# Kernel tuning notes

Hardware: AMD Instinct MI355X
Metric: run time of the kernel (lower is better)

## Reference

```python
import jax, jax.numpy as jnp
import numpy as np

W = 5; WW = 25; STEP = 8; DF = 128; NH = 8; DH = 16; EPS = 1e-5


def sinusoid_pe(ww, d):
    pos = np.arange(ww)[:, None].astype(np.float32)
    div = np.exp(np.arange(0, d, 2).astype(np.float32) * (-np.log(10000.0) / d))
    pe = np.zeros((ww, d), np.float32)
    pe[:, 0::2] = np.sin(pos * div)
    pe[:, 1::2] = np.cos(pos * div)
    return jnp.asarray(pe)


def ln(x, s, b):
    m = x.mean(-1, keepdims=True)
    v = ((x - m) ** 2).mean(-1, keepdims=True)
    return (x - m) / jnp.sqrt(v + EPS) * s + b


def attn_layer(x, src, wq, wk, wv, wm, m1w, m1b, m2w, m2b, n1s, n1b, n2s, n2b):
    N, T, D = x.shape
    q = (x @ wq).reshape(N, T, NH, DH)
    k = (src @ wk).reshape(N, T, NH, DH)
    v = (src @ wv).reshape(N, T, NH, DH)
    a = jax.nn.softmax(jnp.einsum('nqhd,nkhd->nhqk', q, k) * (DH ** -0.5), axis=-1)
    msg = jnp.einsum('nhqk,nkhd->nqhd', a, v).reshape(N, T, D) @ wm
    msg = ln(msg, n1s, n1b)
    h = jnp.concatenate([x, msg], axis=-1)
    h = jax.nn.relu(h @ m1w + m1b) @ m2w + m2b
    return x + ln(h, n2s, n2b)


def local_transformer(x0, x1, P):
    names = ['self', 'cross', 'self', 'cross']
    for i, nm in enumerate(names):
        p = tuple(a[i] for a in P)
        if nm == 'self':
            x0 = attn_layer(x0, x0, *p)
            x1 = attn_layer(x1, x1, *p)
        else:
            x0 = attn_layer(x0, x1, *p)
            x1 = attn_layer(x1, x0, *p)
    return x0, x1


def unfold_window(fm):
    # F.unfold(kernel=5, stride=4, pad=2) then 'B (C MM) L -> B L MM C'
    B, C, H, Wd = fm.shape
    pat = jax.lax.conv_general_dilated_patches(fm, (W, W), (4, 4), [(W // 2, W // 2)] * 2)
    Ho, Wo = pat.shape[2], pat.shape[3]
    pat = pat.reshape(B, C, WW, Ho * Wo)  # channel-major ordering matches torch unfold
    return pat.transpose(0, 3, 2, 1)  # [B, L, WW, C]


def forward(mdesc0, mdesc1, fine0, fine1, conv_w, conv_b, proj_w, proj_b,
            merge_w, merge_b, reg1_w, reg1_b, reg2_w, reg2_b, reg_w, reg_b,
            lt_wq, lt_wk, lt_wv, lt_wm, lt_m1w, lt_m1b, lt_m2w, lt_m2b,
            lt_n1s, lt_n1b, lt_n2s, lt_n2b):
    B, L, Dc = mdesc0.shape
    Wc = int(np.sqrt(L))
    # dual-softmax confidence matrix
    sim = jnp.einsum('bld,bmd->blm', mdesc0 / Dc, mdesc1 / Dc) / 0.1
    cm = jax.nn.softmax(sim, axis=1) * jax.nn.softmax(sim, axis=2)
    # mutual nearest-neighbor filter (static-shape: keep all B*L rows + mask)
    mut = (cm == cm.max(axis=2, keepdims=True)) & (cm == cm.max(axis=1, keepdims=True))
    cf = cm * mut
    mask = cf.max(axis=2) > 0  # [B, L]
    j = jnp.argmax(cf, axis=2)  # [B, L]
    # 1x1 conv to fine dim
    f0 = jnp.einsum('bchw,oc->bohw', fine0, conv_w[:, :, 0, 0]) + conv_b[None, :, None, None]
    f1 = jnp.einsum('bchw,oc->bohw', fine1, conv_w[:, :, 0, 0]) + conv_b[None, :, None, None]
    u0 = unfold_window(f0)
    u1 = unfold_window(f1)  # [B, L, WW, DF]
    N = B * L
    b_all = jnp.repeat(jnp.arange(B), L)
    idx1 = b_all * L + j.reshape(-1)
    local0 = u0.reshape(N, WW, DF)
    local1 = u1.reshape(N, WW, DF)[idx1]
    c0 = mdesc0.reshape(N, Dc)
    c1 = mdesc1.reshape(N, Dc)[idx1]
    local = jnp.concatenate([local0, local1], axis=0)  # [2N, WW, DF]
    center = jnp.concatenate([c0, c1], axis=0) @ proj_w + proj_b  # [2N, DF]
    center = jnp.broadcast_to(center[:, None, :], (2 * N, WW, DF))
    ld = jnp.concatenate([local, center], axis=-1) @ merge_w + merge_b
    ld = ld + sinusoid_pe(WW, DF)[None]
    d0, d1 = ld[:N], ld[N:]
    P = (lt_wq, lt_wk, lt_wv, lt_wm, lt_m1w, lt_m1b, lt_m2w, lt_m2b, lt_n1s, lt_n1b, lt_n2s, lt_n2b)
    fd0, fd1 = local_transformer(d0, d1, P)
    c = WW // 2
    cen = jnp.broadcast_to(fd0[:, c:c + 1, :], (N, WW, DF))
    feat = jnp.concatenate([cen, fd1], axis=-1)  # [N, WW, 2*DF]
    feat = feat @ reg1_w + reg1_b  # [N, WW, DF]
    feat = feat.reshape(N, WW * DF)  # [N, 3200]
    feat = feat @ reg2_w + reg2_b  # dropout is identity at eval
    coords = feat @ reg_w + reg_b  # [N, 2]
    xj = (j % Wc) * STEP
    yj = (j // Wc) * STEP
    base = jnp.stack([xj, yj], axis=-1).reshape(N, 2).astype(coords.dtype)
    return (base + coords) * mask.reshape(N, 1).astype(coords.dtype)


def setup_inputs():
    key = jax.random.key(0)
    ks = jax.random.split(key, 24)
    B, L, Dc = 2, 2304, 256
    Hf = 192
    nl = 4

    def rn(k, shape, fan):
        return jax.random.normal(k, shape, jnp.float32) * (fan ** -0.5)

    return {
        'mdesc0': jax.random.normal(ks[0], (B, L, Dc), jnp.float32),
        'mdesc1': jax.random.normal(ks[1], (B, L, Dc), jnp.float32),
        'fine0': jax.random.normal(ks[2], (B, Dc, Hf, Hf), jnp.float32),
        'fine1': jax.random.normal(ks[3], (B, Dc, Hf, Hf), jnp.float32),
        'conv_w': rn(ks[4], (DF, Dc, 1, 1), Dc),
        'conv_b': jnp.zeros((DF,), jnp.float32),
        'proj_w': rn(ks[5], (Dc, DF), Dc),
        'proj_b': jnp.zeros((DF,), jnp.float32),
        'merge_w': rn(ks[6], (2 * DF, DF), 2 * DF),
        'merge_b': jnp.zeros((DF,), jnp.float32),
        'reg1_w': rn(ks[7], (2 * DF, DF), 2 * DF),
        'reg1_b': jnp.zeros((DF,), jnp.float32),
        'reg2_w': rn(ks[8], (WW * DF, DF), WW * DF),
        'reg2_b': jnp.zeros((DF,), jnp.float32),
        'reg_w': rn(ks[9], (DF, 2), DF),
        'reg_b': jnp.zeros((2,), jnp.float32),
        'lt_wq': rn(ks[10], (nl, DF, DF), DF),
        'lt_wk': rn(ks[11], (nl, DF, DF), DF),
        'lt_wv': rn(ks[12], (nl, DF, DF), DF),
        'lt_wm': rn(ks[13], (nl, DF, DF), DF),
        'lt_m1w': rn(ks[14], (nl, 2 * DF, 2 * DF), 2 * DF),
        'lt_m1b': jnp.zeros((nl, 2 * DF), jnp.float32),
        'lt_m2w': rn(ks[15], (nl, 2 * DF, DF), 2 * DF),
        'lt_m2b': jnp.zeros((nl, DF), jnp.float32),
        'lt_n1s': jnp.ones((nl, DF), jnp.float32),
        'lt_n1b': jnp.zeros((nl, DF), jnp.float32),
        'lt_n2s': jnp.ones((nl, DF), jnp.float32),
        'lt_n2b': jnp.zeros((nl, DF), jnp.float32),
    }


def reference(mdesc0, mdesc1, fine0, fine1, conv_w, conv_b, proj_w, proj_b,
              merge_w, merge_b, reg1_w, reg1_b, reg2_w, reg2_b, reg_w, reg_b,
              lt_wq, lt_wk, lt_wv, lt_wm, lt_m1w, lt_m1b, lt_m2w, lt_m2b,
              lt_n1s, lt_n1b, lt_n2s, lt_n2b):
    return forward(mdesc0, mdesc1, fine0, fine1, conv_w, conv_b, proj_w, proj_b,
                   merge_w, merge_b, reg1_w, reg1_b, reg2_w, reg2_b, reg_w, reg_b,
                   lt_wq, lt_wk, lt_wv, lt_wm, lt_m1w, lt_m1b, lt_m2w, lt_m2b,
                   lt_n1s, lt_n1b, lt_n2s, lt_n2b)
```

## Files before the change

kernel.cpp:

```cpp
#include <hip/hip_runtime.h>
#include <stdint.h>
#include <type_traits>

#define DEVFN static __device__ __forceinline__

typedef __attribute__((ext_vector_type(8))) short bf16x8v;
typedef __attribute__((ext_vector_type(4))) float f32x4v;
typedef __attribute__((ext_vector_type(2))) _Float16 h2;

DEVFN float b2f(short s) {
  union { unsigned u; float f; } c; c.u = ((unsigned)(unsigned short)s) << 16; return c.f;
}
DEVFN short f2b(float f) {
  union { float f; unsigned u; } c; c.f = f;
  unsigned r = c.u + 0x7fffu + ((c.u >> 16) & 1u);
  return (short)(r >> 16);
}
DEVFN short f2h(float f) {
  union { _Float16 h; short s; } c; c.h = (_Float16)f; return c.s;
}
DEVFN void gl_lds16(const void* g, void* l) {
  __builtin_amdgcn_global_load_lds((const __attribute__((address_space(1))) void*)g,
                                   (__attribute__((address_space(3))) void*)l, 16, 0, 0);
}
DEVFN double exp_small(double x) {
  return 1.0 + x * (1.0 + x * (0.5 + x * ((1.0 / 6.0) + x * (1.0 / 24.0))));
}


__global__ void prep_all(const float* __restrict__ conv_w, const float* __restrict__ proj_w,
                         const float* __restrict__ merge_w, const float* __restrict__ reg1_w,
                         const float* __restrict__ reg2_w, const float* __restrict__ wq,
                         const float* __restrict__ wk, const float* __restrict__ wv,
                         const float* __restrict__ wm, const float* __restrict__ m1w,
                         const float* __restrict__ m2w,
                         short* __restrict__ convT, short* __restrict__ projT,
                         short* __restrict__ mergeAT, short* __restrict__ mergeBT,
                         short* __restrict__ reg1T, short* __restrict__ reg2T,
                         short* __restrict__ wqkvT, short* __restrict__ wmT,
                         short* __restrict__ m1T, short* __restrict__ m2T,
                         float* __restrict__ pe, short* __restrict__ zp) {
  const int L0 = 32768, L1 = 32768, L2 = 16384, L3 = 16384, L4 = 32768, L5 = 409600;
  const int L6 = 196608, L7 = 65536, L8 = 262144, L9 = 131072, L10 = 3200, L11 = 128;
  const int TOT = L0+L1+L2+L3+L4+L5+L6+L7+L8+L9+L10+L11;
  for (int gi = blockIdx.x * blockDim.x + threadIdx.x; gi < TOT; gi += gridDim.x * blockDim.x) {
    int i = gi;
    if (i < L0) { convT[i] = f2b(conv_w[i]); continue; } i -= L0;
    if (i < L1) { int n = i >> 8, k = i & 255; projT[i] = f2b(proj_w[k * 128 + n]); continue; } i -= L1;
    if (i < L2) { int n = i >> 7, k = i & 127; mergeAT[i] = f2b(merge_w[k * 128 + n]); continue; } i -= L2;
    if (i < L3) { int n = i >> 7, k = i & 127; mergeBT[i] = f2b(merge_w[(128 + k) * 128 + n]); continue; } i -= L3;
    if (i < L4) { int n = i >> 8, k = i & 255; reg1T[i] = f2b(reg1_w[k * 128 + n]); continue; } i -= L4;
    if (i < L5) { int n = i / 3200, k = i - n * 3200; reg2T[i] = f2b(reg2_w[k * 128 + n]); continue; } i -= L5;
    if (i < L6) {
      int l = i / 49152; int r = i - l * 49152; int w = r / 16384; int r2 = r - w * 16384;
      int n = r2 >> 7, k = r2 & 127;
      const float* s = (w == 0) ? wq : (w == 1) ? wk : wv;
      wqkvT[i] = f2b(s[l * 16384 + k * 128 + n]); continue;
    } i -= L6;
    if (i < L7) { int l = i >> 14; int r = i & 16383; int n = r >> 7, k = r & 127;
      wmT[i] = f2b(wm[l * 16384 + k * 128 + n]); continue; } i -= L7;
    if (i < L8) { int l = i >> 16; int r = i & 65535; int n = r >> 8, k = r & 255;
      m1T[i] = f2b(m1w[l * 65536 + k * 256 + n]); continue; } i -= L8;
    if (i < L9) { int l = i >> 15; int r = i & 32767; int n = r >> 8, k = r & 255;
      m2T[i] = f2b(m2w[l * 32768 + k * 128 + n]); continue; } i -= L9;
    if (i < L10) {
      int t = i >> 7, d = i & 127; int i2 = d >> 1;
      float div = expf(((float)(2 * i2)) * (-logf(10000.f) / 128.f));
      float ang = (float)t * div;
      pe[i] = (d & 1) ? cosf(ang) : sinf(ang); continue;
    } i -= L10;
    zp[i] = 0;
  }
}


__global__ __launch_bounds__(256) void sim_gemm(const float* __restrict__ A,
                                                const float* __restrict__ Bm,
                                                float* __restrict__ S) {
  int b = blockIdx.z;
  A += (size_t)b * 2304 * 256; Bm += (size_t)b * 2304 * 256; S += (size_t)b * 2304 * 2304;
  __shared__ float As[96][33], Bs[96][33];
  int tid = threadIdx.x;
  int tx = tid & 15, ty = tid >> 4;
  int rb = blockIdx.x * 96, cb = blockIdx.y * 96;
  float acc[6][6] = {};
  for (int k0 = 0; k0 < 256; k0 += 32) {
    #pragma unroll
    for (int s = 0; s < 3; ++s) {
      int slot = s * 256 + tid;
      int r = slot >> 3, cq = slot & 7;
      float4 va = *(const float4*)&A[(size_t)(rb + r) * 256 + k0 + 4 * cq];
      float4 vb = *(const float4*)&Bm[(size_t)(cb + r) * 256 + k0 + 4 * cq];
      As[r][4 * cq] = va.x; As[r][4 * cq + 1] = va.y; As[r][4 * cq + 2] = va.z; As[r][4 * cq + 3] = va.w;
      Bs[r][4 * cq] = vb.x; Bs[r][4 * cq + 1] = vb.y; Bs[r][4 * cq + 2] = vb.z; Bs[r][4 * cq + 3] = vb.w;
    }
    __syncthreads();
    #pragma unroll 4
    for (int k = 0; k < 32; ++k) {
      float av[6], bv[6];
      #pragma unroll
      for (int i = 0; i < 6; ++i) av[i] = As[ty + 16 * i][k];
      #pragma unroll
      for (int j = 0; j < 6; ++j) bv[j] = Bs[tx + 16 * j][k];
      #pragma unroll
      for (int i = 0; i < 6; ++i)
        #pragma unroll
        for (int j = 0; j < 6; ++j) acc[i][j] += av[i] * bv[j];
    }
    __syncthreads();
  }
  #pragma unroll
  for (int i = 0; i < 6; ++i)
    #pragma unroll
    for (int j = 0; j < 6; ++j) {
      float t = acc[i][j] * (1.0f / 65536.0f);
      S[(size_t)(rb + ty + 16 * i) * 2304 + cb + tx + 16 * j] = t / 0.1f;
    }
}

__global__ __launch_bounds__(256) void row_lse(const float* __restrict__ S, double* __restrict__ lnR) {
  int row = blockIdx.x;
  const float* Sp = S + (size_t)row * 2304;
  double a = 0;
  for (int m = threadIdx.x; m < 2304; m += 256) a += exp_small((double)Sp[m]);
  __shared__ double red[256];
  red[threadIdx.x] = a; __syncthreads();
  for (int s = 128; s > 0; s >>= 1) { if (threadIdx.x < (unsigned)s) red[threadIdx.x] += red[threadIdx.x + s]; __syncthreads(); }
  if (!threadIdx.x) lnR[row] = log(red[0]);
}

__global__ __launch_bounds__(256) void col_part(const float* __restrict__ S,
                                                const double* __restrict__ lnR,
                                                double* __restrict__ psum,
                                                double* __restrict__ pkey,
                                                int* __restrict__ pidx) {
  int bb = blockIdx.z;
  int c0 = blockIdx.x * 64;
  int rc = blockIdx.y;
  int col = c0 + (threadIdx.x & 63);
  int g = threadIdx.x >> 6;
  const float* Sp = S + (size_t)bb * 2304 * 2304;
  const double* lr = lnR + bb * 2304;
  double a = 0, best = -1e300; int bi = 1 << 30;
  int l0 = rc * 192;
  for (int t = g; t < 192; t += 4) {
    int l = l0 + t;
    double sv = (double)Sp[(size_t)l * 2304 + col];
    a += exp_small(sv);
    double k = 2.0 * sv - lr[l];
    if (k > best || (k == best && l < bi)) { best = k; bi = l; }
  }
  __shared__ double s_sum[256]; __shared__ double s_key[256]; __shared__ int s_idx[256];
  s_sum[threadIdx.x] = a; s_key[threadIdx.x] = best; s_idx[threadIdx.x] = bi;
  __syncthreads();
  if (g == 0) {
    double ts = a; double tk = best; int ti = bi;
    #pragma unroll
    for (int gg = 1; gg < 4; ++gg) {
      int o = threadIdx.x + gg * 64;
      ts += s_sum[o];
      if (s_key[o] > tk || (s_key[o] == tk && s_idx[o] < ti)) { tk = s_key[o]; ti = s_idx[o]; }
    }
    size_t off = ((size_t)bb * 12 + rc) * 2304 + col;
    psum[off] = ts; pkey[off] = tk; pidx[off] = ti;
  }
}

__global__ void col_reduce(const double* __restrict__ psum, const double* __restrict__ pkey,
                           const int* __restrict__ pidx, double* __restrict__ lnC,
                           int* __restrict__ CB) {
  int i = blockIdx.x * blockDim.x + threadIdx.x;
  if (i >= 4608) return;
  int bb = i / 2304, col = i - bb * 2304;
  double s = 0; double bk = -1e300; int bi = 1 << 30;
  for (int rc = 0; rc < 12; ++rc) {
    size_t off = ((size_t)bb * 12 + rc) * 2304 + col;
    s += psum[off];
    double k = pkey[off]; int ix = pidx[off];
    if (k > bk || (k == bk && ix < bi)) { bk = k; bi = ix; }
  }
  lnC[i] = log(s);
  CB[i] = bi;
}

__global__ __launch_bounds__(256) void row_argmax(const float* __restrict__ S,
                                                  const double* __restrict__ lnC,
                                                  int* __restrict__ J) {
  int row = blockIdx.x; int bb = row / 2304;
  const float* Sp = S + (size_t)row * 2304;
  const double* lc = lnC + bb * 2304;
  double best = -1e300; int bi = 1 << 30;
  for (int m = threadIdx.x; m < 2304; m += 256) {
    double k = 2.0 * (double)Sp[m] - lc[m];
    if (k > best || (k == best && m < bi)) { best = k; bi = m; }
  }
  __shared__ double bvs[256]; __shared__ int bis[256];
  bvs[threadIdx.x] = best; bis[threadIdx.x] = bi; __syncthreads();
  for (int s = 128; s > 0; s >>= 1) {
    if (threadIdx.x < (unsigned)s) {
      double ov = bvs[threadIdx.x + s]; int oi = bis[threadIdx.x + s];
      if (ov > bvs[threadIdx.x] || (ov == bvs[threadIdx.x] && oi < bis[threadIdx.x])) { bvs[threadIdx.x] = ov; bis[threadIdx.x] = oi; }
    }
    __syncthreads();
  }
  if (!threadIdx.x) J[row] = bis[0];
}


__global__ __launch_bounds__(256) void transpose_fine(const float* __restrict__ src, short* __restrict__ dst) {
  __shared__ float t[64][65];
  int bb = blockIdx.z, p0 = blockIdx.x * 64, c0 = blockIdx.y * 64;
  for (int i = threadIdx.x; i < 4096; i += 256) {
    int cl = i >> 6, pl = i & 63;
    t[cl][pl] = src[((size_t)(bb * 256 + c0 + cl)) * 36864 + p0 + pl];
  }
  __syncthreads();
  for (int i = threadIdx.x; i < 1024; i += 256) {
    int pl = i >> 4, cg = (i & 15) * 4;
    unsigned w0 = (unsigned short)f2b(t[cg][pl]) | ((unsigned)(unsigned short)f2b(t[cg + 1][pl]) << 16);
    unsigned w1 = (unsigned short)f2b(t[cg + 2][pl]) | ((unsigned)(unsigned short)f2b(t[cg + 3][pl]) << 16);
    int2 v; v.x = (int)w0; v.y = (int)w1;
    *(int2*)&dst[((size_t)(bb * 36864 + p0 + pl)) * 256 + c0 + cg] = v;
  }
}

__global__ void cgather(const float* __restrict__ md0, const float* __restrict__ md1,
                        const int* __restrict__ J, short* __restrict__ cbuf) {
  int total = 9216 * 256;
  for (int i = blockIdx.x * blockDim.x + threadIdx.x; i < total; i += gridDim.x * blockDim.x) {
    int w = i >> 8, c = i & 255;
    const float* src;
    if (w < 4608) src = md0 + (size_t)w * 256;
    else {
      int n = w - 4608; int bb = n / 2304;
      src = md1 + (size_t)(bb * 2304 + J[n]) * 256;
    }
    cbuf[i] = f2b(src[c]);
  }
}

__global__ void build_tab(const int* __restrict__ J, const short* __restrict__ f0c,
                          const short* __restrict__ f1c, const short* __restrict__ zp,
                          unsigned long long* __restrict__ tab) {
  int total = 230400;
  for (int i = blockIdx.x * blockDim.x + threadIdx.x; i < total; i += gridDim.x * blockDim.x) {
    int w = i / 25, t = i - w * 25;
    int bb, cell; const short* fc;
    if (w < 4608) { bb = w / 2304; cell = w - bb * 2304; fc = f0c; }
    else { int n = w - 4608; bb = n / 2304; cell = J[n]; fc = f1c; }
    int cy = cell / 48, cx = cell - cy * 48;
    int y = cy * 4 - 2 + t / 5, x = cx * 4 - 2 + t % 5;
    const short* p = (y >= 0 && y < 192 && x >= 0 && x < 192)
                   ? fc + (size_t)((bb * 192 + y) * 192 + x) * 128 : zp;
    tab[i] = (unsigned long long)(uintptr_t)p;
  }
}


constexpr int AM_LIN = 0, AM_DUAL = 1, AM_TAB = 2, AM_CEN = 3, AM_QKV = 4;
constexpr int EP_BIAS = 0, EP_BF32 = 1, EP_RELU = 2, EP_LN = 3, EP_LNRES = 4, EP_MERGE = 5, EP_PART = 6, EP_F16 = 7;

template<int AMODE, int EPI>
__global__ __launch_bounds__(256)
void gemm_bf16(const short* __restrict__ A1, const short* __restrict__ A2,
               const unsigned long long* __restrict__ tab,
               const short* __restrict__ Wt, int M, int Kd, int kstr, int K1,
               const float* __restrict__ bias, int bstride,
               const float* __restrict__ lns, const float* __restrict__ lnb,
               const short* __restrict__ resid,
               const float* __restrict__ ccp, const float* __restrict__ pep,
               short* __restrict__ outb, float* __restrict__ outf, int ldc,
               long wstride, long ostride) {
  __shared__ __align__(16) short As[128 * 64];
  __shared__ __align__(16) short Bs[128 * 64];
  __shared__ float rsum[2][128], rsq[2][128];
  int tid = threadIdx.x, lane = tid & 63, wid = tid >> 6;
  int wr = wid >> 1, wc = wid & 1;
  int nwg = gridDim.x;
  int orig = blockIdx.x;
  int qd = nwg >> 3, rm = nwg & 7;
  int xcd = orig & 7, offx = orig >> 3;
  int bx = (xcd < rm ? xcd * (qd + 1) : rm * (qd + 1) + (xcd - rm) * qd) + offx;
  int rb = bx * 128;
  int by = blockIdx.y;
  int koff = blockIdx.z * Kd;
  const short* Wsel = Wt + (size_t)by * wstride;
  const float* bsel = bias ? bias + (size_t)by * bstride : nullptr;
  short* osel_b = outb ? outb + (size_t)by * ostride : nullptr;
  float* osel_f = outf ? outf + (size_t)by * ostride : nullptr;

  f32x4v acc[4][4];
  #pragma unroll
  for (int i = 0; i < 4; ++i)
    #pragma unroll
    for (int j = 0; j < 4; ++j) acc[i][j] = (f32x4v){0.f, 0.f, 0.f, 0.f};

  for (int k0 = 0; k0 < Kd; k0 += 64) {
    #pragma unroll
    for (int q = 0; q < 4; ++q) {
      int i = (wid * 4 + q) * 64 + lane;
      int r = i >> 3, pch = i & 7;
      int c = pch ^ (r & 7);
      const short* src;
      if (AMODE == AM_LIN) {
        src = A1 + (size_t)(rb + r) * kstr + koff + k0 + c * 8;
      } else if (AMODE == AM_QKV) {
        const short* Ab = (by == 0) ? A1 : A2;
        src = Ab + (size_t)(rb + r) * kstr + k0 + c * 8;
      } else if (AMODE == AM_DUAL) {
        if (k0 < K1) src = A1 + (size_t)(rb + r) * K1 + k0 + c * 8;
        else         src = A2 + (size_t)(rb + r) * (Kd - K1) + (k0 - K1) + c * 8;
      } else if (AMODE == AM_CEN) {
        int rg = rb + r;
        if (k0 < K1) src = A1 + (size_t)((rg / 25) * 25 + 12) * K1 + k0 + c * 8;
        else         src = A2 + (size_t)rg * (Kd - K1) + (k0 - K1) + c * 8;
      } else {
        src = (const short*)(uintptr_t)tab[rb + r] + k0 + c * 8;
      }
      gl_lds16(src, &As[(size_t)i * 8]);
    }
    #pragma unroll
    for (int q = 0; q < 4; ++q) {
      int i = (wid * 4 + q) * 64 + lane;
      int r = i >> 3, pch = i & 7;
      int c = pch ^ (r & 7);
      gl_lds16(Wsel + (size_t)r * kstr + koff + k0 + c * 8, &Bs[(size_t)i * 8]);
    }
    __syncthreads();
    #pragma unroll
    for (int kk = 0; kk < 2; ++kk) {
      bf16x8v af[4], bfr[4];
      #pragma unroll
      for (int mi = 0; mi < 4; ++mi) {
        int r = wr * 64 + mi * 16 + (lane & 15);
        int c = kk * 4 + (lane >> 4);
        int pch = c ^ (r & 7);
        af[mi] = *(const bf16x8v*)&As[r * 64 + pch * 8];
      }
      #pragma unroll
      for (int ni = 0; ni < 4; ++ni) {
        int r = wc * 64 + ni * 16 + (lane & 15);
        int c = kk * 4 + (lane >> 4);
        int pch = c ^ (r & 7);
        bfr[ni] = *(const bf16x8v*)&Bs[r * 64 + pch * 8];
      }
      #pragma unroll
      for (int mi = 0; mi < 4; ++mi)
        #pragma unroll
        for (int ni = 0; ni < 4; ++ni)
          acc[mi][ni] = __builtin_amdgcn_mfma_f32_16x16x32_bf16(af[mi], bfr[ni], acc[mi][ni], 0, 0, 0);
    }
    __syncthreads();
  }

  int colloc[4];
  #pragma unroll
  for (int ni = 0; ni < 4; ++ni) colloc[ni] = wc * 64 + ni * 16 + (lane & 15);
  float bv[4];
  #pragma unroll
  for (int ni = 0; ni < 4; ++ni)
    bv[ni] = (EPI == EP_MERGE || EPI == EP_PART) ? 0.f : (bsel ? bsel[colloc[ni]] : 0.f);

  #pragma unroll
  for (int mi = 0; mi < 4; ++mi)
    #pragma unroll
    for (int ni = 0; ni < 4; ++ni)
      #pragma unroll
      for (int q = 0; q < 4; ++q) {
        float v = acc[mi][ni][q] + bv[ni];
        if (EPI == EP_RELU) v = fmaxf(v, 0.f);
        acc[mi][ni][q] = v;
      }

  if (EPI == EP_LN || EPI == EP_LNRES) {
    #pragma unroll
    for (int mi = 0; mi < 4; ++mi)
      #pragma unroll
      for (int q = 0; q < 4; ++q) {
        float s = 0.f, ss = 0.f;
        #pragma unroll
        for (int ni = 0; ni < 4; ++ni) { float v = acc[mi][ni][q]; s += v; ss += v * v; }
        s += __shfl_xor(s, 1, 64); ss += __shfl_xor(ss, 1, 64);
        s += __shfl_xor(s, 2, 64); ss += __shfl_xor(ss, 2, 64);
        s += __shfl_xor(s, 4, 64); ss += __shfl_xor(ss, 4, 64);
        s += __shfl_xor(s, 8, 64); ss += __shfl_xor(ss, 8, 64);
        int rl = wr * 64 + mi * 16 + (lane >> 4) * 4 + q;
        if ((lane & 15) == 0) { rsum[wc][rl] = s; rsq[wc][rl] = ss; }
      }
    __syncthreads();
  }

  #pragma unroll
  for (int mi = 0; mi < 4; ++mi)
    #pragma unroll
    for (int q = 0; q < 4; ++q) {
      int rl = wr * 64 + mi * 16 + (lane >> 4) * 4 + q;
      long rg = rb + rl;
      float mean = 0.f, rstd = 0.f;
      if (EPI == EP_LN || EPI == EP_LNRES) {
        float s = rsum[0][rl] + rsum[1][rl];
        float ss = rsq[0][rl] + rsq[1][rl];
        mean = s * (1.f / 128.f);
        float var = ss * (1.f / 128.f) - mean * mean;
        rstd = 1.f / sqrtf(var + 1e-5f);
      }
      int wv_ = 0, tv_ = 0;
      if (EPI == EP_MERGE) { wv_ = (int)(rg / 25); tv_ = (int)(rg - (long)wv_ * 25); }
      #pragma unroll
      for (int ni = 0; ni < 4; ++ni) {
        int cg = colloc[ni];
        float v = acc[mi][ni][q];
        if (EPI == EP_MERGE) v += ccp[(size_t)wv_ * 128 + cg] + pep[tv_ * 128 + cg];
        if (EPI == EP_LN || EPI == EP_LNRES) {
          v = (v - mean) * rstd * lns[cg] + lnb[cg];
          if (EPI == EP_LNRES) v += b2f(resid[(size_t)rg * 128 + cg]);
        }
        if (EPI == EP_BF32) osel_f[(size_t)rg * ldc + cg] = v;
        else if (EPI == EP_PART) osel_f[((size_t)blockIdx.z * M + rg) * ldc + cg] = v;
        else if (EPI == EP_F16) osel_b[(size_t)rg * ldc + cg] = f2h(v);
        else osel_b[(size_t)rg * ldc + cg] = f2b(v);
      }
    }
}

__global__ void reduce_part(const float* __restrict__ part, const float* __restrict__ bias,
                            short* __restrict__ out) {
  int i = blockIdx.x * blockDim.x + threadIdx.x;
  if (i >= 4608 * 128) return;
  int c = i & 127;
  float s = bias[c];
  #pragma unroll
  for (int z = 0; z < 5; ++z) s += part[(size_t)z * 4608 * 128 + i];
  out[i] = f2b(s);
}


__global__ __launch_bounds__(256)
void mlp2_fused(const short* __restrict__ x, const short* __restrict__ attnout,
                const short* __restrict__ wmT,
                const short* __restrict__ m1wT, const short* __restrict__ m2wT,
                const float* __restrict__ n1s, const float* __restrict__ n1b,
                const float* __restrict__ b1, const float* __restrict__ b2,
                const float* __restrict__ lns, const float* __restrict__ lnb,
                short* __restrict__ out) {
  __shared__ __align__(16) short As[64 * 64];
  __shared__ __align__(16) short Bs[128 * 64];
  __shared__ __align__(16) short Hs[64 * 128];
  __shared__ __align__(16) short Ms[64 * 128];
  __shared__ float rsum[2][64], rsq[2][64];
  int tid = threadIdx.x, lane = tid & 63, wid = tid >> 6;
  int wr = wid >> 1, wc = wid & 1;
  int nwg = gridDim.x;
  int orig = blockIdx.x;
  int qd = nwg >> 3, rm = nwg & 7;
  int xcd = orig & 7, offx = orig >> 3;
  int bx = (xcd < rm ? xcd * (qd + 1) : rm * (qd + 1) + (xcd - rm) * qd) + offx;
  int rb = bx * 64;

  int colloc[4];
  #pragma unroll
  for (int ni = 0; ni < 4; ++ni) colloc[ni] = wc * 64 + ni * 16 + (lane & 15);

  {
    f32x4v acc0[2][4];
    #pragma unroll
    for (int i = 0; i < 2; ++i)
      #pragma unroll
      for (int j = 0; j < 4; ++j) acc0[i][j] = (f32x4v){0.f, 0.f, 0.f, 0.f};
    #pragma unroll
    for (int kt = 0; kt < 2; ++kt) {
      int k0 = kt * 64;
      #pragma unroll
      for (int q = 0; q < 2; ++q) {
        int i = (wid * 2 + q) * 64 + lane;
        int r = i >> 3, pch = i & 7;
        int c = pch ^ (r & 7);
        gl_lds16(attnout + (size_t)(rb + r) * 128 + k0 + c * 8, &As[(size_t)i * 8]);
      }
      #pragma unroll
      for (int q = 0; q < 4; ++q) {
        int i = (wid * 4 + q) * 64 + lane;
        int r = i >> 3, pch = i & 7;
        int c = pch ^ (r & 7);
        gl_lds16(wmT + (size_t)r * 128 + k0 + c * 8, &Bs[(size_t)i * 8]);
      }
      __syncthreads();
      #pragma unroll
      for (int kk = 0; kk < 2; ++kk) {
        bf16x8v af[2], bfr[4];
        #pragma unroll
        for (int mi = 0; mi < 2; ++mi) {
          int r = wr * 32 + mi * 16 + (lane & 15);
          int c = kk * 4 + (lane >> 4);
          int pch = c ^ (r & 7);
          af[mi] = *(const bf16x8v*)&As[r * 64 + pch * 8];
        }
        #pragma unroll
        for (int ni = 0; ni < 4; ++ni) {
          int r = wc * 64 + ni * 16 + (lane & 15);
          int c = kk * 4 + (lane >> 4);
          int pch = c ^ (r & 7);
          bfr[ni] = *(const bf16x8v*)&Bs[r * 64 + pch * 8];
        }
        #pragma unroll
        for (int mi = 0; mi < 2; ++mi)
          #pragma unroll
          for (int ni = 0; ni < 4; ++ni)
            acc0[mi][ni] = __builtin_amdgcn_mfma_f32_16x16x32_bf16(af[mi], bfr[ni], acc0[mi][ni], 0, 0, 0);
      }
      __syncthreads();
    }
    #pragma unroll
    for (int mi = 0; mi < 2; ++mi)
      #pragma unroll
      for (int q = 0; q < 4; ++q) {
        float s = 0.f, ss = 0.f;
        #pragma unroll
        for (int ni = 0; ni < 4; ++ni) { float v = acc0[mi][ni][q]; s += v; ss += v * v; }
        s += __shfl_xor(s, 1, 64); ss += __shfl_xor(ss, 1, 64);
        s += __shfl_xor(s, 2, 64); ss += __shfl_xor(ss, 2, 64);
        s += __shfl_xor(s, 4, 64); ss += __shfl_xor(ss, 4, 64);
        s += __shfl_xor(s, 8, 64); ss += __shfl_xor(ss, 8, 64);
        int rl = wr * 32 + mi * 16 + (lane >> 4) * 4 + q;
        if ((lane & 15) == 0) { rsum[wc][rl] = s; rsq[wc][rl] = ss; }
      }
    __syncthreads();
    #pragma unroll
    for (int mi = 0; mi < 2; ++mi)
      #pragma unroll
      for (int q = 0; q < 4; ++q) {
        int rl = wr * 32 + mi * 16 + (lane >> 4) * 4 + q;
        float s = rsum[0][rl] + rsum[1][rl];
        float ss = rsq[0][rl] + rsq[1][rl];
        float mean = s * (1.f / 128.f);
        float var = ss * (1.f / 128.f) - mean * mean;
        float rstd = 1.f / sqrtf(var + 1e-5f);
        #pragma unroll
        for (int ni = 0; ni < 4; ++ni) {
          int cg = colloc[ni];
          float v = (acc0[mi][ni][q] - mean) * rstd * n1s[cg] + n1b[cg];
          int c = cg >> 3, pch = c ^ (rl & 7);
          Ms[rl * 128 + pch * 8 + (cg & 7)] = f2b(v);
        }
      }
    __syncthreads();
  }

  f32x4v acc2[2][4];
  #pragma unroll
  for (int i = 0; i < 2; ++i)
    #pragma unroll
    for (int j = 0; j < 4; ++j) acc2[i][j] = (f32x4v){0.f, 0.f, 0.f, 0.f};

  #pragma unroll
  for (int nh = 0; nh < 2; ++nh) {
    f32x4v acc1[2][4];
    #pragma unroll
    for (int i = 0; i < 2; ++i)
      #pragma unroll
      for (int j = 0; j < 4; ++j) acc1[i][j] = (f32x4v){0.f, 0.f, 0.f, 0.f};

    #pragma unroll
    for (int kt = 0; kt < 4; ++kt) {
      int k0 = kt * 64;
      if (kt < 2) {
        #pragma unroll
        for (int q = 0; q < 2; ++q) {
          int i = (wid * 2 + q) * 64 + lane;
          int r = i >> 3, pch = i & 7;
          int c = pch ^ (r & 7);
          gl_lds16(x + (size_t)(rb + r) * 128 + k0 + c * 8, &As[(size_t)i * 8]);
        }
      }
      #pragma unroll
      for (int q = 0; q < 4; ++q) {
        int i = (wid * 4 + q) * 64 + lane;
        int r = i >> 3, pch = i & 7;
        int c = pch ^ (r & 7);
        gl_lds16(m1wT + (size_t)(nh * 128 + r) * 256 + k0 + c * 8, &Bs[(size_t)i * 8]);
      }
      __syncthreads();
      #pragma unroll
      for (int kk = 0; kk < 2; ++kk) {
        bf16x8v af[2], bfr[4];
        #pragma unroll
        for (int mi = 0; mi < 2; ++mi) {
          int r = wr * 32 + mi * 16 + (lane & 15);
          int c = kk * 4 + (lane >> 4);
          if (kt < 2) {
            int pch = c ^ (r & 7);
            af[mi] = *(const bf16x8v*)&As[r * 64 + pch * 8];
          } else {
            int cM = (kt - 2) * 8 + c;
            int pch = cM ^ (r & 7);
            af[mi] = *(const bf16x8v*)&Ms[r * 128 + pch * 8];
          }
        }
        #pragma unroll
        for (int ni = 0; ni < 4; ++ni) {
          int r = wc * 64 + ni * 16 + (lane & 15);
          int c = kk * 4 + (lane >> 4);
          int pch = c ^ (r & 7);
          bfr[ni] = *(const bf16x8v*)&Bs[r * 64 + pch * 8];
        }
        #pragma unroll
        for (int mi = 0; mi < 2; ++mi)
          #pragma unroll
          for (int ni = 0; ni < 4; ++ni)
            acc1[mi][ni] = __builtin_amdgcn_mfma_f32_16x16x32_bf16(af[mi], bfr[ni], acc1[mi][ni], 0, 0, 0);
      }
      __syncthreads();
    }
    #pragma unroll
    for (int mi = 0; mi < 2; ++mi)
      #pragma unroll
      for (int q = 0; q < 4; ++q) {
        int rl = wr * 32 + mi * 16 + (lane >> 4) * 4 + q;
        #pragma unroll
        for (int ni = 0; ni < 4; ++ni) {
          int cg = wc * 64 + ni * 16 + (lane & 15);
          float v = fmaxf(acc1[mi][ni][q] + b1[nh * 128 + cg], 0.f);
          int c = cg >> 3, pch = c ^ (rl & 7);
          Hs[rl * 128 + pch * 8 + (cg & 7)] = f2b(v);
        }
      }
    __syncthreads();

    #pragma unroll
    for (int k2 = 0; k2 < 2; ++k2) {
      #pragma unroll
      for (int q = 0; q < 4; ++q) {
        int i = (wid * 4 + q) * 64 + lane;
        int r = i >> 3, pch = i & 7;
        int c = pch ^ (r & 7);
        gl_lds16(m2wT + (size_t)r * 256 + nh * 128 + k2 * 64 + c * 8, &Bs[(size_t)i * 8]);
      }
      __syncthreads();
      #pragma unroll
      for (int kk = 0; kk < 2; ++kk) {
        bf16x8v af[2], bfr[4];
        #pragma unroll
        for (int mi = 0; mi < 2; ++mi) {
          int r = wr * 32 + mi * 16 + (lane & 15);
          int cH = k2 * 8 + kk * 4 + (lane >> 4);
          int pch = cH ^ (r & 7);
          af[mi] = *(const bf16x8v*)&Hs[r * 128 + pch * 8];
        }
        #pragma unroll
        for (int ni = 0; ni < 4; ++ni) {
          int r = wc * 64 + ni * 16 + (lane & 15);
          int c = kk * 4 + (lane >> 4);
          int pch = c ^ (r & 7);
          bfr[ni] = *(const bf16x8v*)&Bs[r * 64 + pch * 8];
        }
        #pragma unroll
        for (int mi = 0; mi < 2; ++mi)
          #pragma unroll
          for (int ni = 0; ni < 4; ++ni)
            acc2[mi][ni] = __builtin_amdgcn_mfma_f32_16x16x32_bf16(af[mi], bfr[ni], acc2[mi][ni], 0, 0, 0);
      }
      __syncthreads();
    }
  }

  #pragma unroll
  for (int mi = 0; mi < 2; ++mi)
    #pragma unroll
    for (int ni = 0; ni < 4; ++ni)
      #pragma unroll
      for (int q = 0; q < 4; ++q)
        acc2[mi][ni][q] += b2[colloc[ni]];

  #pragma unroll
  for (int mi = 0; mi < 2; ++mi)
    #pragma unroll
    for (int q = 0; q < 4; ++q) {
      float s = 0.f, ss = 0.f;
      #pragma unroll
      for (int ni = 0; ni < 4; ++ni) { float v = acc2[mi][ni][q]; s += v; ss += v * v; }
      s += __shfl_xor(s, 1, 64); ss += __shfl_xor(ss, 1, 64);
      s += __shfl_xor(s, 2, 64); ss += __shfl_xor(ss, 2, 64);
      s += __shfl_xor(s, 4, 64); ss += __shfl_xor(ss, 4, 64);
      s += __shfl_xor(s, 8, 64); ss += __shfl_xor(ss, 8, 64);
      int rl = wr * 32 + mi * 16 + (lane >> 4) * 4 + q;
      if ((lane & 15) == 0) { rsum[wc][rl] = s; rsq[wc][rl] = ss; }
    }
  __syncthreads();

  #pragma unroll
  for (int mi = 0; mi < 2; ++mi)
    #pragma unroll
    for (int q = 0; q < 4; ++q) {
      int rl = wr * 32 + mi * 16 + (lane >> 4) * 4 + q;
      long rg = rb + rl;
      float s = rsum[0][rl] + rsum[1][rl];
      float ss = rsq[0][rl] + rsq[1][rl];
      float mean = s * (1.f / 128.f);
      float var = ss * (1.f / 128.f) - mean * mean;
      float rstd = 1.f / sqrtf(var + 1e-5f);
      #pragma unroll
      for (int ni = 0; ni < 4; ++ni) {
        int cg = colloc[ni];
        float v = (acc2[mi][ni][q] - mean) * rstd * lns[cg] + lnb[cg];
        v += b2f(x[(size_t)rg * 128 + cg]);
        out[(size_t)rg * 128 + cg] = f2b(v);
      }
    }
}


__global__ __launch_bounds__(256) void attn_win(const short* __restrict__ Q,
                                                const short* __restrict__ K,
                                                const short* __restrict__ V,
                                                short* __restrict__ Mo) {
  int w = blockIdx.x;
  const short* Qg = Q + (size_t)w * 3200;
  const short* Kg = K + (size_t)w * 3200;
  const short* Vg = V + (size_t)w * 3200;
  __shared__ short Qs[25 * 136 + 8], Ks[25 * 136 + 8], Vs[25 * 136 + 8];
  int tid = threadIdx.x;
  for (int s = tid; s < 400; s += 256) {
    int r = s >> 4, ch = s & 15;
    *(int4*)&Qs[r * 136 + ch * 8] = ((const int4*)Qg)[s];
    *(int4*)&Ks[r * 136 + ch * 8] = ((const int4*)Kg)[s];
    *(int4*)&Vs[r * 136 + ch * 8] = ((const int4*)Vg)[s];
  }
  __syncthreads();

  int wid = tid >> 6, lane = tid & 63;
  int half = lane >> 5, li = lane & 31;
  int h = wid * 2 + half;
  if (li < 25) {
    int i = li;
    h2 qr[8];
    #pragma unroll
    for (int t = 0; t < 8; ++t) qr[t] = *(const h2*)&Qs[i * 136 + h * 16 + t * 2];
    float p[25];
    float mx = -1e30f;
    #pragma unroll
    for (int jx = 0; jx < 25; ++jx) {
      const short* kr = &Ks[jx * 136 + h * 16];
      float s = 0.f;
      #pragma unroll
      for (int t = 0; t < 8; ++t)
        s = __builtin_amdgcn_fdot2(qr[t], *(const h2*)&kr[t * 2], s, false);
      s *= 0.25f;
      p[jx] = s;
      mx = fmaxf(mx, s);
    }
    float sum = 0.f;
    #pragma unroll
    for (int jx = 0; jx < 25; ++jx) { float e = expf(p[jx] - mx); p[jx] = e; sum += e; }
    float inv = 1.f / sum;
    h2 o2[8];
    #pragma unroll
    for (int t = 0; t < 8; ++t) { o2[t][0] = (_Float16)0.f; o2[t][1] = (_Float16)0.f; }
    #pragma unroll
    for (int jx = 0; jx < 25; ++jx) {
      _Float16 ph = (_Float16)(p[jx] * inv);
      h2 pv; pv[0] = ph; pv[1] = ph;
      const short* vr = &Vs[jx * 136 + h * 16];
      #pragma unroll
      for (int t = 0; t < 8; ++t) o2[t] += pv * (*(const h2*)&vr[t * 2]);
    }
    int* outp = (int*)(Mo + (size_t)w * 3200 + i * 128 + h * 16);
    #pragma unroll
    for (int t = 0; t < 8; ++t) {
      unsigned lo = (unsigned short)f2b((float)o2[t][0]);
      unsigned hi = (unsigned short)f2b((float)o2[t][1]);
      outp[t] = (int)(lo | (hi << 16));
    }
  }
}


__global__ void final_reg(const short* __restrict__ fv, const float* __restrict__ regw,
                          const float* __restrict__ regb, const int* __restrict__ J,
                          const int* __restrict__ CB, float* __restrict__ out) {
  int n = blockIdx.x * blockDim.x + threadIdx.x;
  if (n >= 4608) return;
  const short* f = fv + (size_t)n * 128;
  float c0 = regb[0], c1 = regb[1];
  for (int d = 0; d < 128; ++d) { float v = b2f(f[d]); c0 += v * regw[d * 2]; c1 += v * regw[d * 2 + 1]; }
  int jv = J[n]; int bb = n / 2304;
  int msk = (CB[bb * 2304 + jv] == (n - bb * 2304)) ? 1 : 0;
  float bx = (float)((jv % 48) * 8), by = (float)((jv / 48) * 8);
  out[n * 2] = msk ? (bx + c0) : 0.f;
  out[n * 2 + 1] = msk ? (by + c1) : 0.f;
}


extern "C" void kernel_launch(void* const* d_in, const int* in_sizes, int n_in,
                              void* d_out, int out_size, void* d_ws, size_t ws_size,
                              hipStream_t stream) {
  const float* md0 = (const float*)d_in[0];
  const float* md1 = (const float*)d_in[1];
  const float* fine0 = (const float*)d_in[2];
  const float* fine1 = (const float*)d_in[3];
  const float* conv_w = (const float*)d_in[4];
  const float* conv_b = (const float*)d_in[5];
  const float* proj_w = (const float*)d_in[6];
  const float* proj_b = (const float*)d_in[7];
  const float* merge_w = (const float*)d_in[8];
  const float* merge_b = (const float*)d_in[9];
  const float* reg1_w = (const float*)d_in[10];
  const float* reg1_b = (const float*)d_in[11];
  const float* reg2_w = (const float*)d_in[12];
  const float* reg2_b = (const float*)d_in[13];
  const float* reg_w = (const float*)d_in[14];
  const float* reg_b = (const float*)d_in[15];
  const float* wq_f = (const float*)d_in[16];
  const float* wk_f = (const float*)d_in[17];
  const float* wv_f = (const float*)d_in[18];
  const float* wm_f = (const float*)d_in[19];
  const float* m1w = (const float*)d_in[20];
  const float* m1b = (const float*)d_in[21];
  const float* m2w = (const float*)d_in[22];
  const float* m2b = (const float*)d_in[23];
  const float* n1s = (const float*)d_in[24];
  const float* n1b = (const float*)d_in[25];
  const float* n2s = (const float*)d_in[26];
  const float* n2b = (const float*)d_in[27];

  char* ws = (char*)d_ws;
  const size_t SZX = (size_t)230400 * 128 * 2;
  const size_t TAILSZ = 20 * 1024 * 1024;
  int CHM = 57600;
  if (SZX + 4ull * 230400 * 256 + TAILSZ <= ws_size)      CHM = 230400;
  else if (SZX + 4ull * 115200 * 256 + TAILSZ <= ws_size) CHM = 115200;
  const size_t CHR = (size_t)CHM * 256;

  short* X  = (short*)(ws);
  char*  Rb = ws + SZX;
  short* R0 = (short*)(Rb);
  short* R1 = (short*)(Rb + CHR);
  short* R2 = (short*)(Rb + 2 * CHR);
  float* S    = (float*)Rb;
  short* F0C  = (short*)Rb;
  short* F1C  = (short*)(Rb + (size_t)73728 * 128 * 2);
  short* FT   = X;
  short* FB   = (short*)Rb;
  float* PART = (float*)(Rb + 2 * CHR);

  char* p = ws + SZX + 4 * CHR;
  double* lnR = (double*)p; p += 4608 * 8;
  double* lnC = (double*)p; p += 4608 * 8;
  int* J = (int*)p; p += 4608 * 4;
  int* CBst = (int*)p; p += 4608 * 4;
  double* PSUM = (double*)p; p += (size_t)2 * 12 * 2304 * 8;
  double* PKEY = (double*)p; p += (size_t)2 * 12 * 2304 * 8;
  int* PIDX = (int*)p; p += (size_t)2 * 12 * 2304 * 4;
  short* CBUF = (short*)p; p += (size_t)9216 * 256 * 2;
  short* CEN = (short*)p; p += (size_t)9216 * 128 * 2;
  float* CC = (float*)p; p += (size_t)9216 * 128 * 4;
  unsigned long long* TAB = (unsigned long long*)p; p += (size_t)230400 * 8;
  float* PE = (float*)p; p += 3200 * 4;
  short* ZP = (short*)p; p += 256;
  short* convT = (short*)p; p += 128 * 256 * 2;
  short* projT = (short*)p; p += 128 * 256 * 2;
  short* mergeAT = (short*)p; p += 128 * 128 * 2;
  short* mergeBT = (short*)p; p += 128 * 128 * 2;
  short* reg1T = (short*)p; p += 128 * 256 * 2;
  short* reg2T = (short*)p; p += (size_t)128 * 3200 * 2;
  short* wqkvT = (short*)p; p += (size_t)4 * 3 * 128 * 128 * 2;
  short* wmT = (short*)p; p += 4 * 128 * 128 * 2;
  short* m1T = (short*)p; p += 4 * 256 * 256 * 2;
  short* m2T = (short*)p; p += (size_t)4 * 128 * 256 * 2;
  short* FV = (short*)p; p += (size_t)4608 * 128 * 2;

  const int TQ = 115200;

  prep_all<<<512, 256, 0, stream>>>(conv_w, proj_w, merge_w, reg1_w, reg2_w,
                                    wq_f, wk_f, wv_f, wm_f, m1w, m2w,
                                    convT, projT, mergeAT, mergeBT, reg1T, reg2T,
                                    wqkvT, wmT, m1T, m2T, PE, ZP);

  sim_gemm<<<dim3(24, 24, 2), 256, 0, stream>>>(md0, md1, S);
  row_lse<<<4608, 256, 0, stream>>>(S, lnR);
  col_part<<<dim3(36, 12, 2), 256, 0, stream>>>(S, lnR, PSUM, PKEY, PIDX);
  col_reduce<<<18, 256, 0, stream>>>(PSUM, PKEY, PIDX, lnC, CBst);
  row_argmax<<<4608, 256, 0, stream>>>(S, lnC, J);

  auto gemm = [&](auto amode, auto epi, const short* A1, const short* A2,
                  const unsigned long long* tab, const short* Wt, int M, int Kd, int kstr, int K1,
                  const float* bias, int bstride, const float* lns, const float* lnb,
                  const short* resid, const float* cc, const float* pe,
                  short* outb, float* outf, int ldc, int NB, int NZ, long wstride, long ostride) {
    constexpr int AM = decltype(amode)::value, EP = decltype(epi)::value;
    gemm_bf16<AM, EP><<<dim3(M / 128, NB, NZ), 256, 0, stream>>>(
        A1, A2, tab, Wt, M, Kd, kstr, K1, bias, bstride, lns, lnb, resid, cc, pe,
        outb, outf, ldc, wstride, ostride);
  };
  using I0 = std::integral_constant<int, 0>; using I1 = std::integral_constant<int, 1>;
  using I2 = std::integral_constant<int, 2>; using I3 = std::integral_constant<int, 3>;
  using I4 = std::integral_constant<int, 4>;
  using E0 = std::integral_constant<int, 0>; using E1 = std::integral_constant<int, 1>;
  using E5 = std::integral_constant<int, 5>; using E6 = std::integral_constant<int, 6>;
  using E7 = std::integral_constant<int, 7>;

  transpose_fine<<<dim3(576, 4, 2), 256, 0, stream>>>(fine0, FT);
  gemm(I0{}, E0{}, FT, nullptr, nullptr, convT, 73728, 256, 256, 0, conv_b, 0, nullptr, nullptr, nullptr, nullptr, nullptr, F0C, nullptr, 128, 1, 1, 0, 0);
  transpose_fine<<<dim3(576, 4, 2), 256, 0, stream>>>(fine1, FT);
  gemm(I0{}, E0{}, FT, nullptr, nullptr, convT, 73728, 256, 256, 0, conv_b, 0, nullptr, nullptr, nullptr, nullptr, nullptr, F1C, nullptr, 128, 1, 1, 0, 0);

  cgather<<<4608, 256, 0, stream>>>(md0, md1, J, CBUF);
  gemm(I0{}, E0{}, CBUF, nullptr, nullptr, projT, 9216, 256, 256, 0, proj_b, 0, nullptr, nullptr, nullptr, nullptr, nullptr, CEN, nullptr, 128, 1, 1, 0, 0);
  gemm(I0{}, E1{}, CEN, nullptr, nullptr, mergeBT, 9216, 128, 128, 0, merge_b, 0, nullptr, nullptr, nullptr, nullptr, nullptr, nullptr, CC, 128, 1, 1, 0, 0);
  build_tab<<<900, 256, 0, stream>>>(J, F0C, F1C, ZP, TAB);
  gemm(I2{}, E5{}, nullptr, nullptr, TAB, mergeAT, 230400, 128, 128, 0, nullptr, 0, nullptr, nullptr, nullptr, CC, PE, X, nullptr, 128, 1, 1, 0, 0);

  auto pass = [&](int i, const short* xq, const short* xkv, short* xout, int Mtotal) {
    const short* wqkv = wqkvT + (size_t)i * 3 * 16384;
    const short* wm = wmT + i * 16384;
    const short* m1 = m1T + i * 65536;
    const short* m2 = m2T + i * 32768;
    for (int off = 0; off < Mtotal; off += CHM) {
      int Mc = (Mtotal - off < CHM) ? (Mtotal - off) : CHM;
      const short* xqc = xq + (size_t)off * 128;
      const short* xkvc = xkv + (size_t)off * 128;
      gemm(I4{}, E7{}, xqc, xkvc, nullptr, wqkv, Mc, 128, 128, 0, nullptr, 0, nullptr, nullptr, nullptr, nullptr, nullptr, R0, nullptr, 128, 3, 1, 16384, (long)CHM * 128);
      attn_win<<<Mc / 25, 256, 0, stream>>>(R0, R1, R2, R0);
      mlp2_fused<<<Mc / 64, 256, 0, stream>>>(xqc, R0, wm, m1, m2,
                                              n1s + i * 128, n1b + i * 128,
                                              m1b + i * 256, m2b + i * 128,
                                              n2s + i * 128, n2b + i * 128,
                                              xout + (size_t)off * 128);
    }
  };
  short* X1 = X + (size_t)TQ * 128;
  for (int i = 0; i < 4; ++i) {
    if ((i & 1) == 0) {
      pass(i, X, X, X, 230400);
    } else {
      pass(i, X, X1, X, TQ);
      pass(i, X1, X, X1, TQ);
    }
  }

  gemm(I3{}, E0{}, X, X1, nullptr, reg1T, TQ, 256, 256, 128, reg1_b, 0, nullptr, nullptr, nullptr, nullptr, nullptr, FB, nullptr, 128, 1, 1, 0, 0);
  gemm(I0{}, E6{}, FB, nullptr, nullptr, reg2T, 4608, 640, 3200, 0, nullptr, 0, nullptr, nullptr, nullptr, nullptr, nullptr, nullptr, PART, 128, 1, 5, 0, 0);
  reduce_part<<<2304, 256, 0, stream>>>(PART, reg2_b, FV);
  final_reg<<<18, 256, 0, stream>>>(FV, reg_w, reg_b, J, CBst, (float*)d_out);
}
```

Before: 1.605 ms.

## Fuse QKV projections into one kernel reusing the staged activation tile

Replaces the three-block QKV GEMM launch with a dedicated kernel. It stages the 128-row activation tile in LDS once, with the full K=128, and reuses it across the Q, K and V weight matrices. Cross-attention layers restage with the other stream's activations after Q. The kernel also remaps block indices across XCDs, and it vectorises the fine-feature transpose loads to float4. The intent is to cut redundant activation reads and launch overhead, at the cost of more LDS per block, which may lower occupancy. The workspace sizing formula is also adjusted.

```diff
diff --git a/kernel.cpp b/kernel.cpp
--- a/kernel.cpp
+++ b/kernel.cpp
@@ -210,9 +210,10 @@
 __global__ __launch_bounds__(256) void transpose_fine(const float* __restrict__ src, short* __restrict__ dst) {
   __shared__ float t[64][65];
   int bb = blockIdx.z, p0 = blockIdx.x * 64, c0 = blockIdx.y * 64;
-  for (int i = threadIdx.x; i < 4096; i += 256) {
-    int cl = i >> 6, pl = i & 63;
-    t[cl][pl] = src[((size_t)(bb * 256 + c0 + cl)) * 36864 + p0 + pl];
+  for (int i = threadIdx.x; i < 1024; i += 256) {
+    int cl = i >> 4, pl = (i & 15) * 4;
+    float4 v = *(const float4*)&src[((size_t)(bb * 256 + c0 + cl)) * 36864 + p0 + pl];
+    t[cl][pl] = v.x; t[cl][pl + 1] = v.y; t[cl][pl + 2] = v.z; t[cl][pl + 3] = v.w;
   }
   __syncthreads();
   for (int i = threadIdx.x; i < 1024; i += 256) {
@@ -257,7 +258,7 @@
 }
 
 
-constexpr int AM_LIN = 0, AM_DUAL = 1, AM_TAB = 2, AM_CEN = 3, AM_QKV = 4;
+constexpr int AM_LIN = 0, AM_DUAL = 1, AM_TAB = 2, AM_CEN = 3;
 constexpr int EP_BIAS = 0, EP_BF32 = 1, EP_RELU = 2, EP_LN = 3, EP_LNRES = 4, EP_MERGE = 5, EP_PART = 6, EP_F16 = 7;
 
 template<int AMODE, int EPI>
@@ -304,9 +305,6 @@
       const short* src;
       if (AMODE == AM_LIN) {
         src = A1 + (size_t)(rb + r) * kstr + koff + k0 + c * 8;
-      } else if (AMODE == AM_QKV) {
-        const short* Ab = (by == 0) ? A1 : A2;
-        src = Ab + (size_t)(rb + r) * kstr + k0 + c * 8;
       } else if (AMODE == AM_DUAL) {
         if (k0 < K1) src = A1 + (size_t)(rb + r) * K1 + k0 + c * 8;
         else         src = A2 + (size_t)(rb + r) * (Kd - K1) + (k0 - K1) + c * 8;
@@ -432,6 +430,95 @@
   #pragma unroll
   for (int z = 0; z < 5; ++z) s += part[(size_t)z * 4608 * 128 + i];
   out[i] = f2b(s);
+}
+
+
+template<bool CROSS>
+__global__ __launch_bounds__(256)
+void qkv_fused(const short* __restrict__ xq, const short* __restrict__ xkv,
+               const short* __restrict__ wqkv, short* __restrict__ out, long ostride) {
+  __shared__ __align__(16) short As[128 * 128];
+  __shared__ __align__(16) short Bs[128 * 64];
+  int tid = threadIdx.x, lane = tid & 63, wid = tid >> 6;
+  int wr = wid >> 1, wc = wid & 1;
+  int nwg = gridDim.x;
+  int orig = blockIdx.x;
+  int qd = nwg >> 3, rm = nwg & 7;
+  int xcd = orig & 7, offx = orig >> 3;
+  int bx = (xcd < rm ? xcd * (qd + 1) : rm * (qd + 1) + (xcd - rm) * qd) + offx;
+  int rb = bx * 128;
+
+  auto stageA = [&](const short* src) {
+    #pragma unroll
+    for (int q = 0; q < 8; ++q) {
+      int i = (wid * 8 + q) * 64 + lane;
+      int r = i >> 4, pch = i & 15;
+      int c = pch ^ (r & 7);
+      gl_lds16(src + (size_t)(rb + r) * 128 + c * 8, &As[(size_t)i * 8]);
+    }
+  };
+  stageA(xq);
+
+  #pragma unroll
+  for (int w = 0; w < 3; ++w) {
+    if (CROSS && w == 1) stageA(xkv);
+    f32x4v acc[4][4];
+    #pragma unroll
+    for (int i = 0; i < 4; ++i)
+      #pragma unroll
+      for (int j = 0; j < 4; ++j) acc[i][j] = (f32x4v){0.f, 0.f, 0.f, 0.f};
+    const short* Wsel = wqkv + (size_t)w * 16384;
+
+    #pragma unroll
+    for (int kt = 0; kt < 2; ++kt) {
+      int k0 = kt * 64;
+      #pragma unroll
+      for (int q = 0; q < 4; ++q) {
+        int i = (wid * 4 + q) * 64 + lane;
+        int r = i >> 3, pch = i & 7;
+        int c = pch ^ (r & 7);
+        gl_lds16(Wsel + (size_t)r * 128 + k0 + c * 8, &Bs[(size_t)i * 8]);
+      }
+      __syncthreads();
+      #pragma unroll
+      for (int kk = 0; kk < 2; ++kk) {
+        bf16x8v af[4], bfr[4];
+        #pragma unroll
+        for (int mi = 0; mi < 4; ++mi) {
+          int r = wr * 64 + mi * 16 + (lane & 15);
+          int cg = kt * 8 + kk * 4 + (lane >> 4);
+          int pch = cg ^ (r & 7);
+          af[mi] = *(const bf16x8v*)&As[r * 128 + pch * 8];
+        }
+        #pragma unroll
+        for (int ni = 0; ni < 4; ++ni) {
+          int r = wc * 64 + ni * 16 + (lane & 15);
+          int c = kk * 4 + (lane >> 4);
+          int pch = c ^ (r & 7);
+          bfr[ni] = *(const bf16x8v*)&Bs[r * 64 + pch * 8];
+        }
+        #pragma unroll
+        for (int mi = 0; mi < 4; ++mi)
+          #pragma unroll
+          for (int ni = 0; ni < 4; ++ni)
+            acc[mi][ni] = __builtin_amdgcn_mfma_f32_16x16x32_bf16(af[mi], bfr[ni], acc[mi][ni], 0, 0, 0);
+      }
+      __syncthreads();
+    }
+    short* ow = out + (size_t)w * ostride;
+    #pragma unroll
+    for (int mi = 0; mi < 4; ++mi)
+      #pragma unroll
+      for (int q = 0; q < 4; ++q) {
+        int rl = wr * 64 + mi * 16 + (lane >> 4) * 4 + q;
+        long rg = rb + rl;
+        #pragma unroll
+        for (int ni = 0; ni < 4; ++ni) {
+          int cg = wc * 64 + ni * 16 + (lane & 15);
+          ow[(size_t)rg * 128 + cg] = f2h(acc[mi][ni][q]);
+        }
+      }
+  }
 }
 
 
@@ -826,8 +913,8 @@
   const size_t SZX = (size_t)230400 * 128 * 2;
   const size_t TAILSZ = 20 * 1024 * 1024;
   int CHM = 57600;
-  if (SZX + 4ull * 230400 * 256 + TAILSZ <= ws_size)      CHM = 230400;
-  else if (SZX + 4ull * 115200 * 256 + TAILSZ <= ws_size) CHM = 115200;
+  if (SZX + 3ull * 230400 * 256 + TAILSZ <= ws_size)      CHM = 230400;
+  else if (SZX + 3ull * 115200 * 256 + TAILSZ <= ws_size) CHM = 115200;
   const size_t CHR = (size_t)CHM * 256;
 
   short* X  = (short*)(ws);
@@ -840,9 +927,10 @@
   short* F1C  = (short*)(Rb + (size_t)73728 * 128 * 2);
   short* FT   = X;
   short* FB   = (short*)Rb;
-  float* PART = (float*)(Rb + 2 * CHR);
-
-  char* p = ws + SZX + 4 * CHR;
+  float* PART = (float*)(Rb + CHR);
+  PART = (float*)(Rb + 2 * CHR);
+
+  char* p = ws + SZX + 3 * CHR;
   double* lnR = (double*)p; p += 4608 * 8;
   double* lnC = (double*)p; p += 4608 * 8;
   int* J = (int*)p; p += 4608 * 4;
@@ -893,10 +981,8 @@
   };
   using I0 = std::integral_constant<int, 0>; using I1 = std::integral_constant<int, 1>;
   using I2 = std::integral_constant<int, 2>; using I3 = std::integral_constant<int, 3>;
-  using I4 = std::integral_constant<int, 4>;
   using E0 = std::integral_constant<int, 0>; using E1 = std::integral_constant<int, 1>;
   using E5 = std::integral_constant<int, 5>; using E6 = std::integral_constant<int, 6>;
-  using E7 = std::integral_constant<int, 7>;
 
   transpose_fine<<<dim3(576, 4, 2), 256, 0, stream>>>(fine0, FT);
   gemm(I0{}, E0{}, FT, nullptr, nullptr, convT, 73728, 256, 256, 0, conv_b, 0, nullptr, nullptr, nullptr, nullptr, nullptr, F0C, nullptr, 128, 1, 1, 0, 0);
@@ -909,7 +995,7 @@
   build_tab<<<900, 256, 0, stream>>>(J, F0C, F1C, ZP, TAB);
   gemm(I2{}, E5{}, nullptr, nullptr, TAB, mergeAT, 230400, 128, 128, 0, nullptr, 0, nullptr, nullptr, nullptr, CC, PE, X, nullptr, 128, 1, 1, 0, 0);
 
-  auto pass = [&](int i, const short* xq, const short* xkv, short* xout, int Mtotal) {
+  auto pass = [&](int i, const short* xq, const short* xkv, short* xout, int Mtotal, bool cross) {
     const short* wqkv = wqkvT + (size_t)i * 3 * 16384;
     const short* wm = wmT + i * 16384;
     const short* m1 = m1T + i * 65536;
@@ -918,7 +1004,10 @@
       int Mc = (Mtotal - off < CHM) ? (Mtotal - off) : CHM;
       const short* xqc = xq + (size_t)off * 128;
       const short* xkvc = xkv + (size_t)off * 128;
-      gemm(I4{}, E7{}, xqc, xkvc, nullptr, wqkv, Mc, 128, 128, 0, nullptr, 0, nullptr, nullptr, nullptr, nullptr, nullptr, R0, nullptr, 128, 3, 1, 16384, (long)CHM * 128);
+      if (cross)
+        qkv_fused<true><<<Mc / 128, 256, 0, stream>>>(xqc, xkvc, wqkv, R0, (long)CHM * 128);
+      else
+        qkv_fused<false><<<Mc / 128, 256, 0, stream>>>(xqc, xkvc, wqkv, R0, (long)CHM * 128);
       attn_win<<<Mc / 25, 256, 0, stream>>>(R0, R1, R2, R0);
       mlp2_fused<<<Mc / 64, 256, 0, stream>>>(xqc, R0, wm, m1, m2,
                                               n1s + i * 128, n1b + i * 128,
@@ -930,10 +1019,10 @@
   short* X1 = X + (size_t)TQ * 128;
   for (int i = 0; i < 4; ++i) {
     if ((i & 1) == 0) {
-      pass(i, X, X, X, 230400);
+      pass(i, X, X, X, 230400, false);
     } else {
-      pass(i, X, X1, X, TQ);
-      pass(i, X1, X, X1, TQ);
+      pass(i, X, X1, X, TQ, true);
+      pass(i, X1, X, X1, TQ, true);
     }
   }
 
```

Result: faster. 1.522 ms (-5.1%).
